# Performance work log

Hardware: AMD Instinct MI355X
Metric: run time of the kernel (lower is better)

Reference implementation:

```python
import jax, jax.numpy as jnp
import numpy as np

N = 100000
E = 3200000
IN_F = 256
OUT_F = 256


def setup_inputs() -> dict:
    key = jax.random.key(0)
    k1, k2, k3, k4, k5 = jax.random.split(key, 5)
    stdv = 1.0 / np.sqrt(OUT_F)
    x = jax.random.normal(k1, (N, IN_F), dtype=jnp.float32)
    edge_index = jax.random.randint(k2, (2, E), 0, N, dtype=jnp.int64)
    edge_weight = jax.random.uniform(k3, (E,), dtype=jnp.float32)
    weight = jax.random.uniform(k4, (IN_F, OUT_F), dtype=jnp.float32, minval=-stdv, maxval=stdv)
    bias = jax.random.uniform(k5, (OUT_F,), dtype=jnp.float32, minval=-stdv, maxval=stdv)
    return {"x": x, "edge_index": edge_index, "edge_weight": edge_weight,
            "weight": weight, "bias": bias}


def reference(x, edge_index, edge_weight, weight, bias):
    # Dense transform: [N, in] @ [in, out] -> [N, out]
    support = x @ weight
    row, col = edge_index[0], edge_index[1]
    # SpMM: out[row] += edge_weight * support[col]
    messages = edge_weight[:, None] * support[col]  # [E, out]
    output = jax.ops.segment_sum(messages, row, num_segments=N)  # [N, out]
    return output + bias
```

## Files before the change

kernel.cpp:

```cpp
#include <hip/hip_runtime.h>
#include <hip/hip_fp16.h>

#define IN_F 256
#define OUT_F 256
#define HALF_F 128
#define RPB_SHIFT 9
#define RPB (1 << RPB_SHIFT)
#define NBINS_MAX 256
#define TILE_E 4096

using bf16x8 = __attribute__((ext_vector_type(8))) short;
using f32x4  = __attribute__((ext_vector_type(4))) float;
using ull    = unsigned long long;

__device__ inline short bf16rne(float f) {
    unsigned u = __float_as_uint(f);
    u = u + 0x7FFFu + ((u >> 16) & 1u);
    return (short)(u >> 16);
}
__device__ inline unsigned pack_half2(float a, float b) {
    __half2 h = __floats2half2_rn(a, b);
    return *reinterpret_cast<unsigned*>(&h);
}

__global__ __launch_bounds__(256) void convert_wt_kernel(
    const float* __restrict__ w, short* __restrict__ wt)
{
    const int idx = blockIdx.x * blockDim.x + threadIdx.x;
    const int c = idx >> 8, k = idx & 255;
    wt[(size_t)c * IN_F + k] = bf16rne(w[(size_t)k * OUT_F + c]);
}

__global__ __launch_bounds__(256) void mfma_gemm_kernel(
    const float* __restrict__ x, const short* __restrict__ wt,
    __half* __restrict__ supA, __half* __restrict__ supB, int M)
{
    const int lane = threadIdx.x & 63;
    const int wid  = threadIdx.x >> 6;
    const int l15  = lane & 15;
    const int l4   = lane >> 4;
    const int rowbase = blockIdx.x * 64;
    const int cbase   = wid * 64;

    f32x4 acc[4][4];
#pragma unroll
    for (int rt = 0; rt < 4; ++rt)
#pragma unroll
        for (int ct = 0; ct < 4; ++ct)
            acc[rt][ct] = (f32x4){0.f, 0.f, 0.f, 0.f};

    const float* xp[4];
    const short* wp[4];
#pragma unroll
    for (int rt = 0; rt < 4; ++rt) {
        int r = rowbase + rt * 16 + l15;
        if (r > M - 1) r = M - 1;
        xp[rt] = x + (size_t)r * IN_F + l4 * 8;
    }
#pragma unroll
    for (int ct = 0; ct < 4; ++ct)
        wp[ct] = wt + (size_t)(cbase + ct * 16 + l15) * IN_F + l4 * 8;

#pragma unroll
    for (int k0 = 0; k0 < IN_F; k0 += 32) {
        bf16x8 b[4];
#pragma unroll
        for (int ct = 0; ct < 4; ++ct)
            b[ct] = *(const bf16x8*)(wp[ct] + k0);

        bf16x8 a[4];
#pragma unroll
        for (int rt = 0; rt < 4; ++rt) {
            const f32x4 f0 = __builtin_nontemporal_load((const f32x4*)(xp[rt] + k0));
            const f32x4 f1 = __builtin_nontemporal_load((const f32x4*)(xp[rt] + k0) + 1);
            bf16x8 v;
            v[0] = bf16rne(f0[0]); v[1] = bf16rne(f0[1]);
            v[2] = bf16rne(f0[2]); v[3] = bf16rne(f0[3]);
            v[4] = bf16rne(f1[0]); v[5] = bf16rne(f1[1]);
            v[6] = bf16rne(f1[2]); v[7] = bf16rne(f1[3]);
            a[rt] = v;
        }

#pragma unroll
        for (int rt = 0; rt < 4; ++rt)
#pragma unroll
            for (int ct = 0; ct < 4; ++ct)
                acc[rt][ct] = __builtin_amdgcn_mfma_f32_16x16x32_bf16(
                    b[ct], a[rt], acc[rt][ct], 0, 0, 0);
    }

    __half* dst = (wid < 2) ? supA : supB;
    const int fbase = (wid & 1) * 64;
#pragma unroll
    for (int rt = 0; rt < 4; ++rt) {
        const int r = rowbase + rt * 16 + l15;
        if (r >= M) continue;
#pragma unroll
        for (int ct = 0; ct < 4; ++ct) {
            uint2 pk;
            pk.x = pack_half2(acc[rt][ct][0], acc[rt][ct][1]);
            pk.y = pack_half2(acc[rt][ct][2], acc[rt][ct][3]);
            *(uint2*)(dst + (size_t)r * HALF_F + fbase + ct * 16 + l4 * 4) = pk;
        }
    }
}

__global__ __launch_bounds__(256) void a1a_hist_kernel(
    const int* __restrict__ ei, int* __restrict__ thist, int E)
{
    __shared__ int hist[NBINS_MAX];
    const int tid = threadIdx.x;
    hist[tid] = 0;
    __syncthreads();
    const int base = blockIdx.x * TILE_E;
#pragma unroll
    for (int i = 0; i < TILE_E / 256; ++i) {
        const int e = base + i * 256 + tid;
        if (e < E)
            atomicAdd(&hist[__builtin_nontemporal_load(ei + e) >> RPB_SHIFT], 1);
    }
    __syncthreads();
    thist[(size_t)blockIdx.x * NBINS_MAX + tid] = hist[tid];
}

__global__ __launch_bounds__(256) void tile_scan_kernel(
    int* __restrict__ thist, int* __restrict__ btot, int T)
{
    const int b   = blockIdx.x;
    const int tid = threadIdx.x;
    __shared__ int s[256];
    int carry = 0;
    for (int c0 = 0; c0 < T; c0 += 256) {
        const int t = c0 + tid;
        const int v = (t < T) ? thist[(size_t)t * NBINS_MAX + b] : 0;
        s[tid] = v;
        __syncthreads();
        for (int d = 1; d < 256; d <<= 1) {
            const int u = (tid >= d) ? s[tid - d] : 0;
            __syncthreads();
            s[tid] += u;
            __syncthreads();
        }
        const int total = s[255];
        if (t < T) thist[(size_t)t * NBINS_MAX + b] = carry + s[tid] - v;
        carry += total;
        __syncthreads();
    }
    if (tid == 0) btot[b] = carry;
}

__global__ __launch_bounds__(NBINS_MAX) void bin_scan_kernel(
    const int* __restrict__ btot, int* __restrict__ bstart, int nbins)
{
    __shared__ int s[NBINS_MAX];
    const int tid = threadIdx.x;
    const int v = (tid < nbins) ? btot[tid] : 0;
    s[tid] = v;
    __syncthreads();
    for (int d = 1; d < NBINS_MAX; d <<= 1) {
        const int u = (tid >= d) ? s[tid - d] : 0;
        __syncthreads();
        s[tid] += u;
        __syncthreads();
    }
    bstart[tid] = s[tid] - v;
}

__global__ __launch_bounds__(256) void a1b_scatter_kernel(
    const int* __restrict__ ei, const float* __restrict__ ew,
    const int* __restrict__ bstart, const int* __restrict__ thist,
    ull* __restrict__ tscw, int E)
{
    __shared__ int hist[NBINS_MAX];
    __shared__ int rbase[NBINS_MAX];
    const int tid = threadIdx.x;
    hist[tid]  = 0;
    rbase[tid] = bstart[tid] + thist[(size_t)blockIdx.x * NBINS_MAX + tid];
    __syncthreads();
    const int base = blockIdx.x * TILE_E;
#pragma unroll
    for (int i = 0; i < TILE_E / 256; ++i) {
        const int e = base + i * 256 + tid;
        if (e < E) {
            const int      row = __builtin_nontemporal_load(ei + e);
            const int      col = __builtin_nontemporal_load(ei + E + e);
            const unsigned wb  = __builtin_nontemporal_load((const unsigned*)ew + e);
            const int b   = row >> RPB_SHIFT;
            const int rnk = atomicAdd(&hist[b], 1);
            tscw[rbase[b] + rnk] = ((ull)wb << 32) |
                                   ((unsigned)col << RPB_SHIFT) |
                                   (unsigned)(row & (RPB - 1));
        }
    }
}

__global__ __launch_bounds__(256) void a2_sort_kernel(
    const ull* __restrict__ tscw, const int* __restrict__ bstart,
    const int* __restrict__ btot, int* __restrict__ counts,
    int* __restrict__ cursor, ull* __restrict__ scw, int M)
{
    const int b   = blockIdx.x;
    const int tid = threadIdx.x;
    const int n   = btot[b];
    const int s0  = bstart[b];

    __shared__ int hist[RPB];
    __shared__ int cur[RPB];
    __shared__ int s[256];

    hist[tid] = 0; hist[tid + 256] = 0;
    __syncthreads();

    for (int i = tid; i < n; i += 256)
        atomicAdd(&hist[(int)(__builtin_nontemporal_load(tscw + s0 + i) & (RPB - 1))], 1);
    __syncthreads();

    const int h0 = hist[2 * tid], h1 = hist[2 * tid + 1];
    const int own = h0 + h1;
    s[tid] = own;
    __syncthreads();
    for (int d = 1; d < 256; d <<= 1) {
        const int u = (tid >= d) ? s[tid - d] : 0;
        __syncthreads();
        s[tid] += u;
        __syncthreads();
    }
    const int excl = s[tid] - own;

    const int r0 = (b << RPB_SHIFT) + 2 * tid, r1 = r0 + 1;
    cur[2 * tid]     = s0 + excl;
    cur[2 * tid + 1] = s0 + excl + h0;
    if (r0 < M) { counts[r0] = h0; cursor[r0] = s0 + excl; }
    if (r1 < M) { counts[r1] = h1; cursor[r1] = s0 + excl + h0; }
    __syncthreads();

    for (int i = tid; i < n; i += 256) {
        const ull en = __builtin_nontemporal_load(tscw + s0 + i);
        const int pos = atomicAdd(&cur[(int)(en & (RPB - 1))], 1);
        scw[pos] = (en & 0xFFFFFFFF00000000ull) |
                   (unsigned)((en >> RPB_SHIFT) & 0x1FFFFu);
    }
}

__global__ __launch_bounds__(256) void pull_half_kernel(
    const int* __restrict__ counts, const int* __restrict__ cursor,
    const ull* __restrict__ scw, const __half* __restrict__ suph,
    const float* __restrict__ biash, float* __restrict__ outh, int M)
{
    const int wv  = blockIdx.x * 4 + (threadIdx.x >> 6);
    const int row = wv * 2 + ((threadIdx.x >> 5) & 1);
    if (row >= M) return;
    const int l = threadIdx.x & 31;

    const int cnt   = counts[row];
    const int start = cursor[row];

    float4 acc = *(const float4*)(biash + l * 4);

#define GATHER_FMA_H(pe)                                                      \
    {                                                                         \
        const int   c  = (int)(unsigned)(pe);                                 \
        const float wj = __uint_as_float((unsigned)((pe) >> 32));             \
        const uint2 v = *(const uint2*)(suph + (size_t)c * HALF_F + l * 4);   \
        const float2 f0 = __half22float2(*(const __half2*)&v.x);              \
        const float2 f1 = __half22float2(*(const __half2*)&v.y);              \
        acc.x = fmaf(wj, f0.x, acc.x); acc.y = fmaf(wj, f0.y, acc.y);         \
        acc.z = fmaf(wj, f1.x, acc.z); acc.w = fmaf(wj, f1.y, acc.w);         \
    }

    for (int j0 = 0; j0 < cnt; j0 += 32) {
        ull pr = 0ull;
        if (j0 + l < cnt)
            pr = __builtin_nontemporal_load(scw + start + j0 + l);
        const int m = min(32, cnt - j0);

        int j = 0;
        for (; j + 4 <= m; j += 4) {
            const ull p0 = __shfl(pr, j, 32),     p1 = __shfl(pr, j + 1, 32);
            const ull p2 = __shfl(pr, j + 2, 32), p3 = __shfl(pr, j + 3, 32);
            GATHER_FMA_H(p0); GATHER_FMA_H(p1);
            GATHER_FMA_H(p2); GATHER_FMA_H(p3);
        }
        for (; j < m; ++j) {
            const ull p = __shfl(pr, j, 32);
            GATHER_FMA_H(p);
        }
    }
#undef GATHER_FMA_H

    f32x4 o; o[0] = acc.x; o[1] = acc.y; o[2] = acc.z; o[3] = acc.w;
    __builtin_nontemporal_store(o, (f32x4*)(outh + (size_t)row * OUT_F + l * 4));
}

__global__ __launch_bounds__(256) void bias_init_kernel(
    float* __restrict__ out, const float* __restrict__ bias, int total4)
{
    const float4* b4 = (const float4*)bias;
    float4* o4 = (float4*)out;
    for (int i = blockIdx.x * blockDim.x + threadIdx.x; i < total4;
         i += gridDim.x * blockDim.x)
        o4[i] = b4[i & 63];
}

__global__ __launch_bounds__(256) void edge_scatter_kernel(
    const int* __restrict__ ei, const float* __restrict__ ew,
    const __half* __restrict__ supA, const __half* __restrict__ supB,
    float* __restrict__ out, int E)
{
    const int e = blockIdx.x * 4 + (threadIdx.x >> 6);
    if (e >= E) return;
    const int lane = threadIdx.x & 63;
    const int   row = ei[e];
    const int   col = ei[E + e];
    const float wgt = ew[e];
    const __half* src = (lane < 32) ? supA : supB;
    const int fl = (lane & 31) * 4;
    const uint2 v = *(const uint2*)(src + (size_t)col * HALF_F + fl);
    const float2 f0 = __half22float2(*(const __half2*)&v.x);
    const float2 f1 = __half22float2(*(const __half2*)&v.y);
    float* o = out + (size_t)row * OUT_F + (lane >> 5) * HALF_F + fl;
    unsafeAtomicAdd(o + 0, wgt * f0.x);
    unsafeAtomicAdd(o + 1, wgt * f0.y);
    unsafeAtomicAdd(o + 2, wgt * f1.x);
    unsafeAtomicAdd(o + 3, wgt * f1.y);
}

extern "C" void kernel_launch(void* const* d_in, const int* in_sizes, int n_in,
                              void* d_out, int out_size, void* d_ws, size_t ws_size,
                              hipStream_t stream)
{
    const float* x    = (const float*)d_in[0];
    const int*   ei   = (const int*)d_in[1];
    const float* ew   = (const float*)d_in[2];
    const float* w    = (const float*)d_in[3];
    const float* bias = (const float*)d_in[4];
    float* out = (float*)d_out;

    const int M = in_sizes[0] / IN_F;
    const int E = in_sizes[2];
    const int nbins = (M + RPB - 1) >> RPB_SHIFT;
    const int T     = (E + TILE_E - 1) / TILE_E;

    char* p = (char*)d_ws;
    const size_t suph_b   = (((size_t)M * HALF_F * sizeof(__half)) + 255) & ~255ull;
    const size_t counts_b = ((size_t)M * 4 + 255) & ~255ull;
    const size_t btot_b   = NBINS_MAX * 4;
    const size_t cursor_b = counts_b;
    const size_t bstart_b = NBINS_MAX * 4;
    const size_t thist_b  = (((size_t)T * NBINS_MAX * 4) + 255) & ~255ull;
    const size_t scw_b    = ((size_t)E * 8 + 255) & ~255ull;
    const size_t tscw_b   = scw_b;
    const size_t wt_b     = (size_t)IN_F * OUT_F * sizeof(short);
    const size_t need     = 2 * suph_b + counts_b + btot_b + cursor_b + bstart_b
                          + thist_b + scw_b + tscw_b + wt_b;

    __half* supA   = (__half*)p;               p += suph_b;
    __half* supB   = (__half*)p;               p += suph_b;
    int*    counts = (int*)p;                  p += counts_b;
    int*    btot   = (int*)p;                  p += btot_b;
    int*    cursor = (int*)p;                  p += cursor_b;
    int*    bstart = (int*)p;                  p += bstart_b;
    int*    thist  = (int*)p;                  p += thist_b;
    ull*    scw    = (ull*)p;                  p += scw_b;
    ull*    tscw   = (ull*)p;                  p += tscw_b;
    short*  wtb    = (short*)p;

    convert_wt_kernel<<<(IN_F * OUT_F) / 256, 256, 0, stream>>>(w, wtb);
    mfma_gemm_kernel<<<(M + 63) / 64, 256, 0, stream>>>(x, wtb, supA, supB, M);

    if (ws_size >= need) {
        a1a_hist_kernel<<<T, 256, 0, stream>>>(ei, thist, E);
        tile_scan_kernel<<<nbins, 256, 0, stream>>>(thist, btot, T);
        bin_scan_kernel<<<1, NBINS_MAX, 0, stream>>>(btot, bstart, nbins);
        a1b_scatter_kernel<<<T, 256, 0, stream>>>(ei, ew, bstart, thist, tscw, E);
        a2_sort_kernel<<<nbins, 256, 0, stream>>>(
            tscw, bstart, btot, counts, cursor, scw, M);
        const int pblocks = ((M + 1) / 2 + 3) / 4;
        pull_half_kernel<<<pblocks, 256, 0, stream>>>(
            counts, cursor, scw, supA, bias, out, M);
        pull_half_kernel<<<pblocks, 256, 0, stream>>>(
            counts, cursor, scw, supB, bias + HALF_F, out + HALF_F, M);
    } else {
        const int total4 = M * OUT_F / 4;
        bias_init_kernel<<<2048, 256, 0, stream>>>(out, bias, total4);
        edge_scatter_kernel<<<(E + 3) / 4, 256, 0, stream>>>(ei, ew, supA, supB, out, E);
    }
}
```

Measured before the change: 471.5 us.

## Stage converted x tile in LDS with double buffering shared across waves

Previously each of the four waves loaded the same 64 rows of x from global memory and converted them to bf16 separately, so x was fetched four times per block. Now each block loads every x chunk once, converts it cooperatively, and stores it in a double-buffered padded LDS tile that all waves read. The next chunk is prefetched into registers while the MFMAs run, which overlaps load latency with compute. The cost is LDS usage plus a __syncthreads per k-step, and the nontemporal load hint is dropped.

```diff
diff --git a/kernel.cpp b/kernel.cpp
--- a/kernel.cpp
+++ b/kernel.cpp
@@ -8,6 +8,7 @@
 #define RPB (1 << RPB_SHIFT)
 #define NBINS_MAX 256
 #define TILE_E 4096
+#define XS_PAD 40
 
 using bf16x8 = __attribute__((ext_vector_type(8))) short;
 using f32x4  = __attribute__((ext_vector_type(4))) float;
@@ -35,13 +36,21 @@
     const float* __restrict__ x, const short* __restrict__ wt,
     __half* __restrict__ supA, __half* __restrict__ supB, int M)
 {
-    const int lane = threadIdx.x & 63;
-    const int wid  = threadIdx.x >> 6;
+    __shared__ short xs[2][64][XS_PAD];
+
+    const int t    = threadIdx.x;
+    const int lane = t & 63;
+    const int wid  = t >> 6;
     const int l15  = lane & 15;
     const int l4   = lane >> 4;
     const int rowbase = blockIdx.x * 64;
     const int cbase   = wid * 64;
 
+    const int srow = t >> 2;
+    const int sks  = (t & 3) * 8;
+    int grow = rowbase + srow; if (grow > M - 1) grow = M - 1;
+    const float* xsrc = x + (size_t)grow * IN_F + sks;
+
     f32x4 acc[4][4];
 #pragma unroll
     for (int rt = 0; rt < 4; ++rt)
@@ -49,37 +58,42 @@
         for (int ct = 0; ct < 4; ++ct)
             acc[rt][ct] = (f32x4){0.f, 0.f, 0.f, 0.f};
 
-    const float* xp[4];
     const short* wp[4];
-#pragma unroll
-    for (int rt = 0; rt < 4; ++rt) {
-        int r = rowbase + rt * 16 + l15;
-        if (r > M - 1) r = M - 1;
-        xp[rt] = x + (size_t)r * IN_F + l4 * 8;
-    }
 #pragma unroll
     for (int ct = 0; ct < 4; ++ct)
         wp[ct] = wt + (size_t)(cbase + ct * 16 + l15) * IN_F + l4 * 8;
 
-#pragma unroll
-    for (int k0 = 0; k0 < IN_F; k0 += 32) {
+    {
+        const float4 f0 = *(const float4*)(xsrc + 0);
+        const float4 f1 = *(const float4*)(xsrc + 4);
+        bf16x8 v;
+        v[0] = bf16rne(f0.x); v[1] = bf16rne(f0.y);
+        v[2] = bf16rne(f0.z); v[3] = bf16rne(f0.w);
+        v[4] = bf16rne(f1.x); v[5] = bf16rne(f1.y);
+        v[6] = bf16rne(f1.z); v[7] = bf16rne(f1.w);
+        *(bf16x8*)&xs[0][srow][sks] = v;
+    }
+    __syncthreads();
+
+#pragma unroll
+    for (int k0 = 0; k0 < 8; ++k0) {
+        const int cur = k0 & 1;
+
+        float4 nf0, nf1;
+        if (k0 < 7) {
+            nf0 = *(const float4*)(xsrc + (k0 + 1) * 32);
+            nf1 = *(const float4*)(xsrc + (k0 + 1) * 32 + 4);
+        }
+
         bf16x8 b[4];
 #pragma unroll
         for (int ct = 0; ct < 4; ++ct)
-            b[ct] = *(const bf16x8*)(wp[ct] + k0);
+            b[ct] = *(const bf16x8*)(wp[ct] + k0 * 32);
 
         bf16x8 a[4];
 #pragma unroll
-        for (int rt = 0; rt < 4; ++rt) {
-            const f32x4 f0 = __builtin_nontemporal_load((const f32x4*)(xp[rt] + k0));
-            const f32x4 f1 = __builtin_nontemporal_load((const f32x4*)(xp[rt] + k0) + 1);
-            bf16x8 v;
-            v[0] = bf16rne(f0[0]); v[1] = bf16rne(f0[1]);
-            v[2] = bf16rne(f0[2]); v[3] = bf16rne(f0[3]);
-            v[4] = bf16rne(f1[0]); v[5] = bf16rne(f1[1]);
-            v[6] = bf16rne(f1[2]); v[7] = bf16rne(f1[3]);
-            a[rt] = v;
-        }
+        for (int rt = 0; rt < 4; ++rt)
+            a[rt] = *(const bf16x8*)&xs[cur][rt * 16 + l15][l4 * 8];
 
 #pragma unroll
         for (int rt = 0; rt < 4; ++rt)
@@ -87,6 +101,16 @@
             for (int ct = 0; ct < 4; ++ct)
                 acc[rt][ct] = __builtin_amdgcn_mfma_f32_16x16x32_bf16(
                     b[ct], a[rt], acc[rt][ct], 0, 0, 0);
+
+        if (k0 < 7) {
+            bf16x8 v;
+            v[0] = bf16rne(nf0.x); v[1] = bf16rne(nf0.y);
+            v[2] = bf16rne(nf0.z); v[3] = bf16rne(nf0.w);
+            v[4] = bf16rne(nf1.x); v[5] = bf16rne(nf1.y);
+            v[6] = bf16rne(nf1.z); v[7] = bf16rne(nf1.w);
+            *(bf16x8*)&xs[cur ^ 1][srow][sks] = v;
+        }
+        __syncthreads();
     }
 
     __half* dst = (wid < 2) ? supA : supB;
```

Result: faster. 413.2 us (-12.4%).
